# Optimization experiments

Measured on AMD Instinct MI355X. Metric: run time of the kernel, lower is better.

The kernel has to match this reference:

```python
import jax, jax.numpy as jnp
import numpy as np

NUM_HEADS = 16
HEAD_DIM = 64


def setup_inputs() -> dict:
    key = jax.random.key(0)
    k1, k2, k3 = jax.random.split(key, 3)
    dim = NUM_HEADS * HEAD_DIM  # 1024
    x = jax.random.normal(k1, (1, 4096, dim), dtype=jnp.float32)
    w_qkv = jax.random.normal(k2, (dim, 3 * dim), dtype=jnp.float32) * (dim ** -0.5)
    w_out = jax.random.normal(k3, (dim, dim), dtype=jnp.float32) * (dim ** -0.5)
    b_out = jnp.zeros((dim,), dtype=jnp.float32)
    return {"x": x, "w_qkv": w_qkv, "w_out": w_out, "b_out": b_out}


def reference(x, w_qkv, w_out, b_out):
    b, n, dim = x.shape
    h, d = NUM_HEADS, HEAD_DIM
    qkv = x @ w_qkv                                  # [b, n, 3*h*d]
    q, k, v = jnp.split(qkv, 3, axis=-1)
    q = q.reshape(b, n, h, d)
    k = k.reshape(b, n, h, d)
    v = v.reshape(b, n, h, d)  # NOTE: unused below — source module's bug uses K as V
    q = q * (d ** -0.5)
    # The chunked online-softmax in the source is mathematically exact softmax
    # attention; express it directly. Scores layout matches einsum '...qhd,...khd->...qhk'.
    scores = jnp.einsum('bqhd,bkhd->bqhk', q, k)     # [b, n, h, n]
    attn = jax.nn.softmax(scores, axis=-1)
    # Faithful to source bug: value_chunk was sliced from `key`, so V := K here.
    att = jnp.einsum('bqhk,bkhd->bqhd', attn, k)     # [b, n, h, d]
    out = att.reshape(b, n, h * d)
    return out @ w_out + b_out
```

## Files before the change

### kernel.cpp

```cpp
#include <hip/hip_runtime.h>
#include <hip/hip_bf16.h>

#define NT 4096
#define DIM 1024
#define NH 16
#define HD 64

typedef __attribute__((ext_vector_type(8))) short bf16x8;
typedef __attribute__((ext_vector_type(4))) float f32x4;
typedef __attribute__((ext_vector_type(16))) float f32x16;

__device__ __forceinline__ unsigned short f2b(float f) {
  union { float f; unsigned u; } v; v.f = f;
  unsigned r = v.u + 0x7fffu + ((v.u >> 16) & 1u);
  return (unsigned short)(r >> 16);
}

__device__ __forceinline__ float fexp2(float x) {
#if __has_builtin(__builtin_amdgcn_exp2f)
  return __builtin_amdgcn_exp2f(x);
#else
  return exp2f(x);
#endif
}

__global__ void k_cvt(const float4* __restrict__ src, ushort4* __restrict__ dst, int n4) {
  int i = blockIdx.x * blockDim.x + threadIdx.x;
  if (i >= n4) return;
  float4 v = src[i];
  ushort4 o;
  o.x = f2b(v.x); o.y = f2b(v.y); o.z = f2b(v.z); o.w = f2b(v.w);
  dst[i] = o;
}

__global__ __launch_bounds__(256) void k_trans_w(const float* __restrict__ src, int S,
                                                 unsigned short* __restrict__ dst, int Kdim) {
  __shared__ float tile[32][33];
  int j0 = blockIdx.x * 32, k0 = blockIdx.y * 32;
  int t = threadIdx.x;
  int c = t & 31, rq = t >> 5;
#pragma unroll
  for (int i = 0; i < 4; i++) {
    int r = rq + i * 8;
    tile[r][c] = src[(size_t)(k0 + r) * S + j0 + c];
  }
  __syncthreads();
#pragma unroll
  for (int i = 0; i < 4; i++) {
    int jr = rq + i * 8;
    dst[(size_t)(j0 + jr) * Kdim + k0 + c] = f2b(tile[c][jr]);
  }
}

template <int EPI>
__global__ __launch_bounds__(256) void k_gemm(const unsigned short* __restrict__ A,
                                              const unsigned short* __restrict__ Bt,
                                              unsigned short* __restrict__ qh,
                                              unsigned short* __restrict__ krm,
                                              float* __restrict__ cout,
                                              const float* __restrict__ bias) {
  __shared__ unsigned short As[128][40];
  __shared__ unsigned short Bs[128][40];
  const int K = 1024;
  int m0 = blockIdx.y * 128, n0 = blockIdx.x * 128;
  int t = threadIdx.x;
  int w = t >> 6, l = t & 63;
  int wr = w >> 1, wc = w & 1;
  int lq = l & 15, lg = l >> 4;
  f32x4 zero = {0.f, 0.f, 0.f, 0.f};
  f32x4 acc[4][4];
#pragma unroll
  for (int i = 0; i < 4; i++)
#pragma unroll
    for (int j = 0; j < 4; j++) acc[i][j] = zero;

  for (int k0 = 0; k0 < K; k0 += 32) {
#pragma unroll
    for (int s = 0; s < 2; s++) {
      int slot = t + s * 256;
      int r = slot >> 2, c8 = (slot & 3) * 8;
      *reinterpret_cast<bf16x8*>(&As[r][c8]) =
          *reinterpret_cast<const bf16x8*>(A + (size_t)(m0 + r) * K + k0 + c8);
      *reinterpret_cast<bf16x8*>(&Bs[r][c8]) =
          *reinterpret_cast<const bf16x8*>(Bt + (size_t)(n0 + r) * K + k0 + c8);
    }
    __syncthreads();
    bf16x8 af[4], bf[4];
#pragma unroll
    for (int mi = 0; mi < 4; mi++)
      af[mi] = *reinterpret_cast<bf16x8*>(&As[wr * 64 + mi * 16 + lq][lg * 8]);
#pragma unroll
    for (int ni = 0; ni < 4; ni++)
      bf[ni] = *reinterpret_cast<bf16x8*>(&Bs[wc * 64 + ni * 16 + lq][lg * 8]);
#pragma unroll
    for (int mi = 0; mi < 4; mi++)
#pragma unroll
      for (int ni = 0; ni < 4; ni++)
        acc[mi][ni] =
            __builtin_amdgcn_mfma_f32_16x16x32_bf16(af[mi], bf[ni], acc[mi][ni], 0, 0, 0);
    __syncthreads();
  }
#pragma unroll
  for (int mi = 0; mi < 4; mi++) {
#pragma unroll
    for (int ni = 0; ni < 4; ni++) {
      int j = n0 + wc * 64 + ni * 16 + lq;
#pragma unroll
      for (int r = 0; r < 4; r++) {
        int row = m0 + wr * 64 + mi * 16 + lg * 4 + r;
        float v = acc[mi][ni][r];
        if (EPI == 0) {
          if (j < DIM) {
            qh[((size_t)(j >> 6) << 18) + (size_t)row * HD + (j & 63)] =
                f2b(v * 0.18033688011112042f);
          } else {
            int jj = j - DIM;
            krm[((size_t)(jj >> 6) << 18) + (size_t)row * HD + (jj & 63)] = f2b(v);
          }
        } else {
          cout[(size_t)row * DIM + j] = v + bias[j];
        }
      }
    }
  }
}

__global__ __launch_bounds__(256) void k_transK(const unsigned short* __restrict__ krm,
                                                unsigned short* __restrict__ kt) {
  __shared__ unsigned short tile[64][72];
  int h = blockIdx.y, n0 = blockIdx.x * 64;
  int t = threadIdx.x;
  const unsigned short* src = krm + (size_t)h * NT * HD;
#pragma unroll
  for (int s = 0; s < 2; s++) {
    int slot = t + s * 256;
    int r = slot >> 3, c8 = (slot & 7) * 8;
    *reinterpret_cast<bf16x8*>(&tile[r][c8]) =
        *reinterpret_cast<const bf16x8*>(src + (size_t)(n0 + r) * HD + c8);
  }
  __syncthreads();
  unsigned short* dst = kt + (size_t)h * HD * NT;
#pragma unroll
  for (int s = 0; s < 2; s++) {
    int slot = t + s * 256;
    int dd = slot & 63, c8 = (slot >> 6) * 8;
    bf16x8 vv;
#pragma unroll
    for (int i = 0; i < 8; i++) vv[i] = (short)tile[c8 + i][dd];
    *reinterpret_cast<bf16x8*>(dst + (size_t)dd * NT + n0 + c8) = vv;
  }
}

__global__ __launch_bounds__(256) void k_attn(const unsigned short* __restrict__ qh,
                                              const unsigned short* __restrict__ krm,
                                              const unsigned short* __restrict__ kt,
                                              unsigned short* __restrict__ att) {
  __shared__ __align__(16) unsigned char sbuf[2][16384];

  int hw = blockIdx.x;
  int xcd = hw & 7, idx = hw >> 3;
  int h = xcd * 2 + (idx >> 5);
  int q0 = (idx & 31) * 128;

  int t = threadIdx.x, w = t >> 6, l = t & 63;
  int lq = l & 31, hi = l >> 5;
  const unsigned char* Kb = (const unsigned char*)(krm + (size_t)h * NT * HD);
  const unsigned char* Tb = (const unsigned char*)(kt + (size_t)h * HD * NT);
  const unsigned short* Qb = qh + (size_t)h * NT * HD;

  int qrow = q0 + w * 32 + lq;
  bf16x8 qf[4];
#pragma unroll
  for (int ds = 0; ds < 4; ds++)
    qf[ds] = *reinterpret_cast<const bf16x8*>(Qb + (size_t)qrow * HD + ds * 16 + hi * 8);

  int swz = (lq & 7) << 4;
  int qk_off[2][4], pv_off[2][4];
#pragma unroll
  for (int kb2 = 0; kb2 < 2; kb2++)
#pragma unroll
    for (int ds = 0; ds < 4; ds++)
      qk_off[kb2][ds] = ((kb2 * 32 + lq) << 7) + ((32 * ds + 16 * hi) ^ swz);
#pragma unroll
  for (int dblk = 0; dblk < 2; dblk++)
#pragma unroll
    for (int kb = 0; kb < 4; kb++)
      pv_off[dblk][kb] = 8192 + ((dblk * 32 + lq) << 7) + ((32 * kb + 16 * hi) ^ swz);

  f32x16 o0, o1;
#pragma unroll
  for (int r = 0; r < 16; r++) { o0[r] = 0.f; o1[r] = 0.f; }
  float m_run = -3.0e38f, l_run = 0.f;

  auto STAGE = [&](int b, int kv0) {
    unsigned char* base = &sbuf[b][0];
#pragma unroll
    for (int i = 0; i < 4; i++) {
      int c = w * 4 + i;
      int o = c * 1024 + l * 16;
      const unsigned char* g;
      if (c < 8) {
        int row = o >> 7;
        int so = (o ^ ((row & 7) << 4)) & 127;
        g = Kb + (size_t)(kv0 + row) * 128 + so;
      } else {
        int oo = o - 8192;
        int row = oo >> 7;
        int so = (oo ^ ((row & 7) << 4)) & 127;
        g = Tb + (size_t)row * 8192 + (size_t)kv0 * 2 + so;
      }
      __builtin_amdgcn_global_load_lds(
          (const __attribute__((address_space(1))) unsigned int*)g,
          (__attribute__((address_space(3))) unsigned int*)(base + c * 1024), 16, 0, 0);
    }
  };

  STAGE(0, 0);
  __syncthreads();

  for (int tile = 0; tile < 64; tile++) {
    int cur = tile & 1;
    if (tile < 63) STAGE(cur ^ 1, (tile + 1) * 64);
    const unsigned char* KaB = &sbuf[cur][0];

    f32x16 s0, s1;
#pragma unroll
    for (int r = 0; r < 16; r++) { s0[r] = 0.f; s1[r] = 0.f; }
#pragma unroll
    for (int ds = 0; ds < 4; ds++) {
      bf16x8 a0 = *reinterpret_cast<const bf16x8*>(KaB + qk_off[0][ds]);
      bf16x8 a1 = *reinterpret_cast<const bf16x8*>(KaB + qk_off[1][ds]);
      s0 = __builtin_amdgcn_mfma_f32_32x32x16_bf16(a0, qf[ds], s0, 0, 0, 0);
      s1 = __builtin_amdgcn_mfma_f32_32x32x16_bf16(a1, qf[ds], s1, 0, 0, 0);
    }

    float pm = -3.0e38f;
#pragma unroll
    for (int r = 0; r < 16; r++) pm = fmaxf(pm, fmaxf(s0[r], s1[r]));
    pm = fmaxf(pm, __shfl_xor(pm, 32));
    if (__any(pm > m_run + 8.0f)) {
      float newm = fmaxf(m_run, pm);
      float al = fexp2(m_run - newm);
#pragma unroll
      for (int r = 0; r < 16; r++) {
        float av = __shfl(al, (r & 3) + 8 * (r >> 2) + 4 * hi);
        o0[r] *= av;
        o1[r] *= av;
      }
      l_run *= al;
      m_run = newm;
    }
    float p0[16], p1[16];
    float ps = 0.f;
#pragma unroll
    for (int r = 0; r < 16; r++) { p0[r] = fexp2(s0[r] - m_run); ps += p0[r]; }
#pragma unroll
    for (int r = 0; r < 16; r++) { p1[r] = fexp2(s1[r] - m_run); ps += p1[r]; }
    ps += __shfl_xor(ps, 32);
    l_run += ps;

    unsigned pk0[8], pk1[8];
#pragma unroll
    for (int i = 0; i < 8; i++) {
      asm("v_cvt_pk_bf16_f32 %0, %1, %2" : "=v"(pk0[i]) : "v"(p0[2 * i]), "v"(p0[2 * i + 1]));
      asm("v_cvt_pk_bf16_f32 %0, %1, %2" : "=v"(pk1[i]) : "v"(p1[2 * i]), "v"(p1[2 * i + 1]));
    }
    bf16x8 pf[4];
#pragma unroll
    for (int kb = 0; kb < 4; kb++) {
      const unsigned* pk = (kb < 2) ? pk0 : pk1;
      int m = kb & 1;
      unsigned d0 = pk[4 * m + 0], d1 = pk[4 * m + 1];
      unsigned e0 = pk[4 * m + 2], e1 = pk[4 * m + 3];
      asm volatile("v_permlane32_swap_b32 %0, %1" : "+v"(d0), "+v"(e0));
      asm volatile("v_permlane32_swap_b32 %0, %1" : "+v"(d1), "+v"(e1));
      union { unsigned u[4]; bf16x8 v; } uu;
      uu.u[0] = d0; uu.u[1] = d1; uu.u[2] = e0; uu.u[3] = e1;
      pf[kb] = uu.v;
    }

#pragma unroll
    for (int kb = 0; kb < 4; kb++) {
      bf16x8 v0 = *reinterpret_cast<const bf16x8*>(KaB + pv_off[0][kb]);
      o0 = __builtin_amdgcn_mfma_f32_32x32x16_bf16(pf[kb], v0, o0, 0, 0, 0);
    }
#pragma unroll
    for (int kb = 0; kb < 4; kb++) {
      bf16x8 v1 = *reinterpret_cast<const bf16x8*>(KaB + pv_off[1][kb]);
      o1 = __builtin_amdgcn_mfma_f32_32x32x16_bf16(pf[kb], v1, o1, 0, 0, 0);
    }
    __syncthreads();
  }

  float linv = 1.0f / l_run;
#pragma unroll
  for (int r = 0; r < 16; r++) {
    int qr = (r & 3) + 8 * (r >> 2) + 4 * hi;
    float lv = __shfl(linv, qr);
    size_t grow = (size_t)(q0 + w * 32 + qr);
    att[grow * DIM + h * HD + lq] = f2b(o0[r] * lv);
    att[grow * DIM + h * HD + 32 + lq] = f2b(o1[r] * lv);
  }
}

extern "C" void kernel_launch(void* const* d_in, const int* in_sizes, int n_in,
                              void* d_out, int out_size, void* d_ws, size_t ws_size,
                              hipStream_t stream) {
  const float* x = (const float*)d_in[0];
  const float* w_qkv = (const float*)d_in[1];
  const float* w_out = (const float*)d_in[2];
  const float* b_out = (const float*)d_in[3];
  float* out = (float*)d_out;

  char* ws = (char*)d_ws;
  unsigned short* xb   = (unsigned short*)(ws);
  unsigned short* wqkT = (unsigned short*)(ws + 8388608);
  unsigned short* woT  = (unsigned short*)(ws + 12582912);
  unsigned short* qhb  = (unsigned short*)(ws + 14680064);
  unsigned short* krm  = (unsigned short*)(ws + 23068672);
  unsigned short* ktb  = (unsigned short*)(ws + 31457280);
  unsigned short* attb = (unsigned short*)(ws + 39845888);

  k_cvt<<<(NT * DIM / 4 + 255) / 256, 256, 0, stream>>>((const float4*)x, (ushort4*)xb,
                                                        NT * DIM / 4);
  dim3 g1(2048 / 32, 1024 / 32);
  k_trans_w<<<g1, 256, 0, stream>>>(w_qkv, 3 * DIM, wqkT, DIM);
  dim3 g2(1024 / 32, 1024 / 32);
  k_trans_w<<<g2, 256, 0, stream>>>(w_out, DIM, woT, DIM);
  dim3 g3(2048 / 128, NT / 128);
  k_gemm<0><<<g3, 256, 0, stream>>>(xb, wqkT, qhb, krm, nullptr, nullptr);
  dim3 g4(NT / 64, NH);
  k_transK<<<g4, 256, 0, stream>>>(krm, ktb);
  k_attn<<<(NT / 128) * NH, 256, 0, stream>>>(qhb, krm, ktb, attb);
  dim3 g5(DIM / 128, NT / 128);
  k_gemm<1><<<g5, 256, 0, stream>>>(attb, woT, nullptr, nullptr, out, b_out);
}
```

Baseline: 181.6 us.

## Split attention KV range in two and merge partials with combine kernel

Attention is now split-K: each block processes half of the key/value sequence, doubling the grid from 512 to 1024 blocks, and writes unnormalized bf16 partial outputs plus per-row running max and sum. A new combine kernel rescales and merges the two partials into the attention buffer. This is meant to raise occupancy and balance across the GPU's compute units, at the cost of an extra kernel launch, additional memory traffic, and bf16 rounding of the unnormalized partials. Workspace buffers (xb and wqkT) are reused for the partials and stats after the GEMM that needs them has run.

```diff
diff --git a/kernel.cpp b/kernel.cpp
--- a/kernel.cpp
+++ b/kernel.cpp
@@ -14,6 +14,9 @@
   union { float f; unsigned u; } v; v.f = f;
   unsigned r = v.u + 0x7fffu + ((v.u >> 16) & 1u);
   return (unsigned short)(r >> 16);
+}
+__device__ __forceinline__ float b2f(unsigned short u) {
+  union { unsigned u; float f; } v; v.u = ((unsigned)u) << 16; return v.f;
 }
 
 __device__ __forceinline__ float fexp2(float x) {
@@ -154,13 +157,22 @@
 __global__ __launch_bounds__(256) void k_attn(const unsigned short* __restrict__ qh,
                                               const unsigned short* __restrict__ krm,
                                               const unsigned short* __restrict__ kt,
-                                              unsigned short* __restrict__ att) {
+                                              unsigned short* __restrict__ part0,
+                                              unsigned short* __restrict__ part1,
+                                              float* __restrict__ stats) {
   __shared__ __align__(16) unsigned char sbuf[2][16384];
 
   int hw = blockIdx.x;
   int xcd = hw & 7, idx = hw >> 3;
-  int h = xcd * 2 + (idx >> 5);
-  int q0 = (idx & 31) * 128;
+  int h = xcd * 2 + (idx >> 6);
+  int sub = idx & 63;
+  int q0 = (sub & 31) * 128;
+  int kvs = sub >> 5;
+  int kv_base = kvs * (NT / 2);
+
+  unsigned short* ob = kvs ? part1 : part0;
+  float* mb = stats + (size_t)kvs * 2 * (NH * NT);
+  float* lb = mb + NH * NT;
 
   int t = threadIdx.x, w = t >> 6, l = t & 63;
   int lq = l & 31, hi = l >> 5;
@@ -215,12 +227,12 @@
     }
   };
 
-  STAGE(0, 0);
+  STAGE(0, kv_base);
   __syncthreads();
 
-  for (int tile = 0; tile < 64; tile++) {
+  for (int tile = 0; tile < 32; tile++) {
     int cur = tile & 1;
-    if (tile < 63) STAGE(cur ^ 1, (tile + 1) * 64);
+    if (tile < 31) STAGE(cur ^ 1, kv_base + (tile + 1) * 64);
     const unsigned char* KaB = &sbuf[cur][0];
 
     f32x16 s0, s1;
@@ -292,15 +304,45 @@
     __syncthreads();
   }
 
-  float linv = 1.0f / l_run;
 #pragma unroll
   for (int r = 0; r < 16; r++) {
     int qr = (r & 3) + 8 * (r >> 2) + 4 * hi;
-    float lv = __shfl(linv, qr);
     size_t grow = (size_t)(q0 + w * 32 + qr);
-    att[grow * DIM + h * HD + lq] = f2b(o0[r] * lv);
-    att[grow * DIM + h * HD + 32 + lq] = f2b(o1[r] * lv);
-  }
+    ob[grow * DIM + h * HD + lq] = f2b(o0[r]);
+    ob[grow * DIM + h * HD + 32 + lq] = f2b(o1[r]);
+  }
+  if (l < 32) {
+    int q = q0 + w * 32 + lq;
+    mb[h * NT + q] = m_run;
+    lb[h * NT + q] = l_run;
+  }
+}
+
+__global__ __launch_bounds__(256) void k_combine(unsigned short* __restrict__ p0b,
+                                                 const unsigned short* __restrict__ p1b,
+                                                 const float* __restrict__ stats) {
+  int i = blockIdx.x * 256 + threadIdx.x;
+  int base = i * 8;
+  int q = base >> 10;
+  int c = base & 1023;
+  int h = c >> 6;
+  const float* m0 = stats;
+  const float* l0 = stats + NH * NT;
+  const float* m1 = stats + 2 * NH * NT;
+  const float* l1 = stats + 3 * NH * NT;
+  float mm0 = m0[h * NT + q], ll0 = l0[h * NT + q];
+  float mm1 = m1[h * NT + q], ll1 = l1[h * NT + q];
+  float M = fmaxf(mm0, mm1);
+  float s0 = fexp2(mm0 - M), s1 = fexp2(mm1 - M);
+  float dn = ll0 * s0 + ll1 * s1;
+  float a0 = s0 / dn, a1 = s1 / dn;
+  bf16x8 v0 = *reinterpret_cast<const bf16x8*>(p0b + base);
+  bf16x8 v1 = *reinterpret_cast<const bf16x8*>(p1b + base);
+  bf16x8 o;
+#pragma unroll
+  for (int j = 0; j < 8; j++)
+    o[j] = (short)f2b(b2f((unsigned short)v0[j]) * a0 + b2f((unsigned short)v1[j]) * a1);
+  *reinterpret_cast<bf16x8*>(p0b + base) = o;
 }
 
 extern "C" void kernel_launch(void* const* d_in, const int* in_sizes, int n_in,
@@ -320,6 +362,7 @@
   unsigned short* krm  = (unsigned short*)(ws + 23068672);
   unsigned short* ktb  = (unsigned short*)(ws + 31457280);
   unsigned short* attb = (unsigned short*)(ws + 39845888);
+  float* stats = (float*)wqkT;
 
   k_cvt<<<(NT * DIM / 4 + 255) / 256, 256, 0, stream>>>((const float4*)x, (ushort4*)xb,
                                                         NT * DIM / 4);
@@ -331,7 +374,8 @@
   k_gemm<0><<<g3, 256, 0, stream>>>(xb, wqkT, qhb, krm, nullptr, nullptr);
   dim3 g4(NT / 64, NH);
   k_transK<<<g4, 256, 0, stream>>>(krm, ktb);
-  k_attn<<<(NT / 128) * NH, 256, 0, stream>>>(qhb, krm, ktb, attb);
+  k_attn<<<(NT / 128) * NH * 2, 256, 0, stream>>>(qhb, krm, ktb, attb, xb, stats);
+  k_combine<<<NT * DIM / 8 / 256, 256, 0, stream>>>(attb, xb, stats);
   dim3 g5(DIM / 128, NT / 128);
   k_gemm<1><<<g5, 256, 0, stream>>>(attb, woT, nullptr, nullptr, out, b_out);
 }
```

After: 188.2 us. 3.6% more time.
